# Optimization experiments

Hardware: AMD Instinct MI355X
Metric: run time of the kernel (lower is better)

## Reference

```python
import jax, jax.numpy as jnp
import numpy as np

N_SRC0, N_DST0, N_DST1 = 400000, 200000, 100000
E0, E1 = 3200000, 1600000
IN_FEATS, H_FEATS, NUM_CLASSES, NUM_CELL_TYPES = 128, 256, 8, 24


def setup_inputs() -> dict:
    key = jax.random.key(0)
    ks = jax.random.split(key, 12)
    feats = jax.random.normal(ks[0], (N_SRC0, IN_FEATS), dtype=jnp.float32)
    cell_ids = jax.random.randint(ks[1], (N_SRC0,), 0, NUM_CELL_TYPES)
    x = jnp.concatenate([cell_ids.astype(jnp.float32)[:, None], feats], axis=1)  # [N,129]
    src0 = jax.random.randint(ks[2], (E0,), 0, N_SRC0, dtype=jnp.int32)
    dst0 = jax.random.randint(ks[3], (E0,), 0, N_DST0, dtype=jnp.int32)
    src1 = jax.random.randint(ks[4], (E1,), 0, N_DST0, dtype=jnp.int32)
    dst1 = jax.random.randint(ks[5], (E1,), 0, N_DST1, dtype=jnp.int32)
    s = 1.0 / np.sqrt(IN_FEATS)
    s2 = 1.0 / np.sqrt(H_FEATS)
    return {
        "x": x,
        "src0": src0, "dst0": dst0, "src1": src1, "dst1": dst1,
        "n_dst0": N_DST0, "n_dst1": N_DST1,
        "emb": jax.random.normal(ks[6], (NUM_CELL_TYPES, IN_FEATS), dtype=jnp.float32),
        "W_self1": jax.random.normal(ks[7], (IN_FEATS, H_FEATS), dtype=jnp.float32) * s,
        "W_neigh1": jax.random.normal(ks[8], (IN_FEATS, H_FEATS), dtype=jnp.float32) * s,
        "b1": jnp.zeros((H_FEATS,), dtype=jnp.float32),
        "W_self2": jax.random.normal(ks[9], (H_FEATS, NUM_CLASSES), dtype=jnp.float32) * s2,
        "W_neigh2": jax.random.normal(ks[10], (H_FEATS, NUM_CLASSES), dtype=jnp.float32) * s2,
        "b2": jnp.zeros((NUM_CLASSES,), dtype=jnp.float32),
    }


def _sage_mean(h_src, h_dst, src, dst, n_dst, W_self, W_neigh, b):
    # gather src features along edges, mean-reduce onto dst nodes
    msg = h_src[src]                                                # [E, d]
    agg = jax.ops.segment_sum(msg, dst, num_segments=n_dst)        # [n_dst, d]
    deg = jax.ops.segment_sum(jnp.ones_like(dst, dtype=h_src.dtype), dst, num_segments=n_dst)
    agg = agg / jnp.maximum(deg, 1.0)[:, None]
    return h_dst @ W_self + agg @ W_neigh + b


def reference(x, src0, dst0, src1, dst1, n_dst0, n_dst1,
              emb, W_self1, W_neigh1, b1, W_self2, W_neigh2, b2):
    cell_ids = x[:, 0].astype(jnp.int32)
    feat = x[:, 1:]
    h = feat * jax.nn.sigmoid(emb[cell_ids])  # embedding-gated features; dropout = identity (eval)
    h_dst = h[:n_dst0]
    h1 = jax.nn.relu(_sage_mean(h, h_dst, src0, dst0, n_dst0, W_self1, W_neigh1, b1))
    h1_dst = h1[:n_dst1]
    out = _sage_mean(h1, h1_dst, src1, dst1, n_dst1, W_self2, W_neigh2, b2)
    return out
```

## Files before the change

kernel.cpp:

```cpp
#include <hip/hip_runtime.h>

typedef unsigned int uint;
typedef unsigned short ushort;
typedef __attribute__((ext_vector_type(8))) short short8;
typedef __attribute__((ext_vector_type(4))) float f32x4;

__device__ __forceinline__ float bflo(uint u) { return __uint_as_float(u << 16); }
__device__ __forceinline__ float bfhi(uint u) { return __uint_as_float(u & 0xffff0000u); }
__device__ __forceinline__ ushort f2bf(float f) {
    uint u = __float_as_uint(f);
    u += 0x7fffu + ((u >> 16) & 1u);
    return (ushort)(u >> 16);
}
__device__ __forceinline__ uint pack2(float a, float b) {
    return (uint)f2bf(a) | ((uint)f2bf(b) << 16);
}
__device__ __forceinline__ float sigm(float e) { return 1.0f / (1.0f + __expf(-e)); }

#define ND0 200000
#define ND1 100000
#define INF 128
#define HF  256
#define BCAP 24576
#define GSTRIDE 16

__global__ __launch_bounds__(256) void gate_k(const float* __restrict__ x,
                                              const float* __restrict__ emb,
                                              ushort* __restrict__ h, int nnodes) {
    int tid  = blockIdx.x * 256 + threadIdx.x;
    int node = tid >> 4, tq = tid & 15;
    if (node >= nnodes) return;
    const float* xr = x + (size_t)node * 129;
    int cell = (int)xr[0];
    int f0 = tq * 8;
    const float* er = emb + cell * INF + f0;
    float4 e0 = *(const float4*)er;
    float4 e1 = *(const float4*)(er + 4);
    float v[8];
    __builtin_memcpy(&v[0], xr + 1 + f0, 16);
    __builtin_memcpy(&v[4], xr + 5 + f0, 16);
    uint4 o;
    o.x = pack2(v[0] * sigm(e0.x), v[1] * sigm(e0.y));
    o.y = pack2(v[2] * sigm(e0.z), v[3] * sigm(e0.w));
    o.z = pack2(v[4] * sigm(e1.x), v[5] * sigm(e1.y));
    o.w = pack2(v[6] * sigm(e1.z), v[7] * sigm(e1.w));
    *(uint4*)(h + (size_t)node * INF + f0) = o;
}

#define SCAN_B 1024
__global__ __launch_bounds__(256) void scan1_k(const int* __restrict__ in,
                                               int* __restrict__ out,
                                               int* __restrict__ bsum, int n) {
    __shared__ int tmp[256];
    int t = threadIdx.x;
    int base = blockIdx.x * SCAN_B;
    int v[4], s = 0;
#pragma unroll
    for (int q = 0; q < 4; ++q) {
        int idx = base + t * 4 + q;
        v[q] = (idx < n) ? ((in[idx] + 3) & ~3) : 0;
        s += v[q];
    }
    tmp[t] = s; __syncthreads();
    for (int off = 1; off < 256; off <<= 1) {
        int xv = (t >= off) ? tmp[t - off] : 0; __syncthreads();
        tmp[t] += xv; __syncthreads();
    }
    int excl = tmp[t] - s;
#pragma unroll
    for (int q = 0; q < 4; ++q) {
        int idx = base + t * 4 + q;
        if (idx < n) out[idx] = excl;
        excl += v[q];
    }
    if (t == 255) bsum[blockIdx.x] = tmp[255];
}

__global__ __launch_bounds__(256) void scan2_k(int* __restrict__ bsum, int nb) {
    __shared__ int tmp[256];
    int t = threadIdx.x;
    int s = (t < nb) ? bsum[t] : 0;
    tmp[t] = s; __syncthreads();
    for (int off = 1; off < 256; off <<= 1) {
        int xv = (t >= off) ? tmp[t - off] : 0; __syncthreads();
        tmp[t] += xv; __syncthreads();
    }
    if (t < nb) bsum[t] = tmp[t] - s;
}

__global__ __launch_bounds__(256) void scan3_k(int* __restrict__ row_start,
                                               const int* __restrict__ bsum, int n) {
    int i = blockIdx.x * blockDim.x + threadIdx.x;
    if (i < n) row_start[i] += bsum[i >> 10];
}

#define CHUNK_A 2048
__global__ __launch_bounds__(256) void binA_k(const int* __restrict__ src,
                                              const int* __restrict__ dst,
                                              uint* __restrict__ pairs,
                                              int* __restrict__ gcur,
                                              int* __restrict__ cnt, int E) {
    __shared__ int hist[256];
    __shared__ int base[256];
    int t = threadIdx.x;
    for (int c0 = blockIdx.x * CHUNK_A; c0 < E; c0 += gridDim.x * CHUNK_A) {
        int n = min(CHUNK_A, E - c0);
        hist[t] = 0;
        __syncthreads();
        int i0 = t * 8;
        uint meta[8];
        if (i0 + 8 <= n) {
            int4 da = *(const int4*)(dst + c0 + i0);
            int4 db = *(const int4*)(dst + c0 + i0 + 4);
            int dv[8] = { da.x, da.y, da.z, da.w, db.x, db.y, db.z, db.w };
#pragma unroll
            for (int q = 0; q < 8; ++q) {
                int d = dv[q];
                atomicAdd(&cnt[d], 1);
                int b = d >> 10;
                int r = atomicAdd(&hist[b], 1);
                meta[q] = ((uint)b << 21) | ((uint)r << 10) | (uint)(d & 1023);
            }
        } else {
#pragma unroll
            for (int q = 0; q < 8; ++q) {
                int i = i0 + q;
                if (i < n) {
                    int d = dst[c0 + i];
                    atomicAdd(&cnt[d], 1);
                    int b = d >> 10;
                    int r = atomicAdd(&hist[b], 1);
                    meta[q] = ((uint)b << 21) | ((uint)r << 10) | (uint)(d & 1023);
                } else meta[q] = 0xFFFFFFFFu;
            }
        }
        __syncthreads();
        base[t] = hist[t] ? atomicAdd(&gcur[t * GSTRIDE], hist[t]) : 0;
        __syncthreads();
        if (i0 + 8 <= n) {
            int4 sa = *(const int4*)(src + c0 + i0);
            int4 sb = *(const int4*)(src + c0 + i0 + 4);
            int sv[8] = { sa.x, sa.y, sa.z, sa.w, sb.x, sb.y, sb.z, sb.w };
#pragma unroll
            for (int q = 0; q < 8; ++q) {
                uint m = meta[q];
                uint b = m >> 21;
                uint p = (uint)base[b] + ((m >> 10) & 2047u);
                pairs[(size_t)b * BCAP + p] = ((uint)sv[q] << 10) | (m & 1023u);
            }
        } else {
#pragma unroll
            for (int q = 0; q < 8; ++q) {
                uint m = meta[q];
                if (m != 0xFFFFFFFFu) {
                    uint b = m >> 21;
                    uint p = (uint)base[b] + ((m >> 10) & 2047u);
                    pairs[(size_t)b * BCAP + p] = ((uint)src[c0 + i0 + q] << 10) | (m & 1023u);
                }
            }
        }
        __syncthreads();
    }
}

__global__ __launch_bounds__(1024) void binB_k(const uint* __restrict__ pairs,
                                               const int* __restrict__ gcur,
                                               const int* __restrict__ row_start,
                                               int* __restrict__ csr, int nd, int zrow) {
    __shared__ int cur[1024];
    int b = blockIdx.x, t = threadIdx.x;
    int dbase = b << 10;
    cur[t] = (dbase + t < nd) ? row_start[dbase + t] : 0;
    __syncthreads();
    int ne = gcur[b * GSTRIDE];
    const uint* bp = pairs + (size_t)b * BCAP;
    for (int i = t; i < ne; i += 1024) {
        uint e = bp[i];
        int p = atomicAdd(&cur[e & 1023], 1);
        csr[p] = (int)(e >> 10);
    }
    __syncthreads();
    if (dbase + t < nd) {
        int pe = cur[t];
        int pad = (-(pe - row_start[dbase + t])) & 3;
        for (int q = 0; q < pad; ++q) csr[pe + q] = zrow;
    }
}

__global__ __launch_bounds__(256) void gather4_k(const int* __restrict__ csr,
                                                 const int* __restrict__ row_start,
                                                 const int* __restrict__ cnt,
                                                 const ushort* __restrict__ hsrc,
                                                 uint* __restrict__ aggm, int nrows) {
    int w    = (blockIdx.x * blockDim.x + threadIdx.x) >> 6;
    int lane = threadIdx.x & 63;
    if (w >= nrows) return;
    int beg = row_start[w], c = cnt[w];
    int end = beg + ((c + 3) & ~3);
    const uint* hb = (const uint*)hsrc;
    float a0 = 0.f, a1 = 0.f;
    for (int j = beg; j < end; j += 4) {
        int4 s4 = *(const int4*)(csr + j);
        uint u0 = hb[(size_t)s4.x * 64 + lane];
        uint u1 = hb[(size_t)s4.y * 64 + lane];
        uint u2 = hb[(size_t)s4.z * 64 + lane];
        uint u3 = hb[(size_t)s4.w * 64 + lane];
        a0 += (bflo(u0) + bflo(u1)) + (bflo(u2) + bflo(u3));
        a1 += (bfhi(u0) + bfhi(u1)) + (bfhi(u2) + bfhi(u3));
    }
    float inv = 1.0f / fmaxf((float)c, 1.0f);
    aggm[(size_t)w * 64 + lane] = pack2(a0 * inv, a1 * inv);
}

__global__ __launch_bounds__(256) void wconv_k(const float* __restrict__ Ws,
                                               const float* __restrict__ Wn,
                                               uint* __restrict__ Wb) {
    int tid  = blockIdx.x * 256 + threadIdx.x;
    int lane = tid & 63, nf = (tid >> 6) & 15, ks = tid >> 10;
    int n  = nf * 16 + (lane & 15);
    int k0 = ks * 32 + ((lane >> 4) << 3);
    uint o[4];
#pragma unroll
    for (int p = 0; p < 4; ++p) {
        int k = k0 + 2 * p;
        float a = (k < 128)     ? Ws[(size_t)k * HF + n]       : Wn[(size_t)(k - 128) * HF + n];
        float b = (k + 1 < 128) ? Ws[(size_t)(k + 1) * HF + n] : Wn[(size_t)(k - 127) * HF + n];
        o[p] = pack2(a, b);
    }
    uint4 v = { o[0], o[1], o[2], o[3] };
    *(uint4*)(Wb + (size_t)tid * 4) = v;
}

__global__ __launch_bounds__(256) void wpack2_k(const float* __restrict__ Ws2,
                                                const float* __restrict__ Wn2,
                                                uint* __restrict__ Wb2) {
    int tid = blockIdx.x * 256 + threadIdx.x;
    if (tid >= 512) return;
    int lane = tid & 63, ks = tid >> 6;
    int n  = lane & 15;
    int k0 = ks * 32 + ((lane >> 4) << 3);
    const float* W = (n < 8) ? Wn2 : Ws2;
    int c = n & 7;
    uint o[4];
#pragma unroll
    for (int p = 0; p < 4; ++p) {
        int k = k0 + 2 * p;
        o[p] = pack2(W[(size_t)k * 8 + c], W[(size_t)(k + 1) * 8 + c]);
    }
    uint4 v = { o[0], o[1], o[2], o[3] };
    *(uint4*)(Wb2 + (size_t)tid * 4) = v;
}

__global__ __launch_bounds__(256) void layer1_mfma_k(const uint* __restrict__ hb,
                                                     const uint* __restrict__ aggm,
                                                     const uint* __restrict__ Wb,
                                                     const uint* __restrict__ Wb2,
                                                     const float* __restrict__ b1,
                                                     float* __restrict__ z,
                                                     float* __restrict__ out, int nd1) {
    __shared__ uint lds[64 * 132];
    int t = threadIdx.x, lane = t & 63, wid = t >> 6;
    int quad = lane >> 4, l16 = lane & 15;
    int r0 = blockIdx.x * 64;

#pragma unroll
    for (int it = 0; it < 8; ++it) {
        int i = t + it * 256;
        int r = i >> 5, u4 = i & 31;
        const uint* src = (u4 < 16) ? (hb + (size_t)(r0 + r) * 64 + u4 * 4)
                                    : (aggm + (size_t)(r0 + r) * 64 + (u4 - 16) * 4);
        *(uint4*)&lds[r * 132 + u4 * 4] = *(const uint4*)src;
    }

    float bias[4];
#pragma unroll
    for (int i = 0; i < 4; ++i) bias[i] = b1[wid * 64 + i * 16 + l16];
    f32x4 acc[4][4];
#pragma unroll
    for (int mf = 0; mf < 4; ++mf)
#pragma unroll
        for (int i = 0; i < 4; ++i)
            acc[mf][i] = (f32x4){ bias[i], bias[i], bias[i], bias[i] };

    __syncthreads();

#pragma unroll
    for (int ks = 0; ks < 8; ++ks) {
        short8 bfr[4];
#pragma unroll
        for (int i = 0; i < 4; ++i) {
            int nf = wid * 4 + i;
            bfr[i] = *(const short8*)(Wb + (size_t)((ks * 16 + nf) * 64 + lane) * 4);
        }
        short8 afr[4];
#pragma unroll
        for (int mf = 0; mf < 4; ++mf) {
            int r = mf * 16 + l16;
            afr[mf] = *(const short8*)&lds[r * 132 + ks * 16 + quad * 4];
        }
#pragma unroll
        for (int mf = 0; mf < 4; ++mf)
#pragma unroll
            for (int i = 0; i < 4; ++i)
                acc[mf][i] = __builtin_amdgcn_mfma_f32_16x16x32_bf16(afr[mf], bfr[i],
                                                                     acc[mf][i], 0, 0, 0);
    }

    __syncthreads();
    ushort* st = (ushort*)lds;
#pragma unroll
    for (int mf = 0; mf < 4; ++mf)
#pragma unroll
        for (int i = 0; i < 4; ++i) {
            int col = wid * 64 + i * 16 + l16;
#pragma unroll
            for (int reg = 0; reg < 4; ++reg) {
                int row = mf * 16 + quad * 4 + reg;
                st[row * 264 + col] = f2bf(fmaxf(acc[mf][i][reg], 0.0f));
            }
        }
    __syncthreads();

    f32x4 zacc = (f32x4){ 0.f, 0.f, 0.f, 0.f };
    int rloc = wid * 16 + l16;
#pragma unroll
    for (int ks = 0; ks < 8; ++ks) {
        short8 a = *(const short8*)&lds[rloc * 132 + ks * 16 + quad * 4];
        short8 b = *(const short8*)(Wb2 + (size_t)(ks * 64 + lane) * 4);
        zacc = __builtin_amdgcn_mfma_f32_16x16x32_bf16(a, b, zacc, 0, 0, 0);
    }
#pragma unroll
    for (int reg = 0; reg < 4; ++reg) {
        int r = r0 + wid * 16 + quad * 4 + reg;
        if (l16 < 8) z[(size_t)r * 8 + l16] = zacc[reg];
        else if (r < nd1) out[(size_t)r * 8 + (l16 - 8)] = zacc[reg];
    }
}

__global__ __launch_bounds__(256) void gz_k(const int* __restrict__ csr,
                                            const int* __restrict__ row_start,
                                            const int* __restrict__ cnt,
                                            const float* __restrict__ z,
                                            const float* __restrict__ b2,
                                            float* __restrict__ out, int nrows) {
    int tid = blockIdx.x * 256 + threadIdx.x;
    int d = tid >> 3, c = tid & 7;
    if (d >= nrows) return;
    int beg = row_start[d], n = cnt[d];
    int end = beg + ((n + 3) & ~3);
    float a = 0.f;
    for (int j = beg; j < end; j += 4) {
        int4 s4 = *(const int4*)(csr + j);
        a += z[(size_t)s4.x * 8 + c] + z[(size_t)s4.y * 8 + c]
           + z[(size_t)s4.z * 8 + c] + z[(size_t)s4.w * 8 + c];
    }
    float inv = 1.0f / fmaxf((float)n, 1.0f);
    out[(size_t)d * 8 + c] += a * inv + b2[c];
}

extern "C" void kernel_launch(void* const* d_in, const int* in_sizes, int n_in,
                              void* d_out, int out_size, void* d_ws, size_t ws_size,
                              hipStream_t stream) {
    const float* x    = (const float*)d_in[0];
    const int*   src0 = (const int*)d_in[1];
    const int*   dst0 = (const int*)d_in[2];
    const int*   src1 = (const int*)d_in[3];
    const int*   dst1 = (const int*)d_in[4];
    const float* emb  = (const float*)d_in[7];
    const float* Ws1  = (const float*)d_in[8];
    const float* Wn1  = (const float*)d_in[9];
    const float* b1   = (const float*)d_in[10];
    const float* Ws2  = (const float*)d_in[11];
    const float* Wn2  = (const float*)d_in[12];
    const float* b2   = (const float*)d_in[13];
    int E0 = in_sizes[1];
    int E1 = in_sizes[3];
    int nsrc = in_sizes[0] / 129;

    char* p = (char*)d_ws;
    ushort* h         = (ushort*)p;  p += ((size_t)nsrc + 1) * INF * 2;
    uint*   aggm      = (uint*)p;    p += (size_t)ND0 * 64 * 4;
    int*    csr       = (int*)p;     p += ((size_t)E0 + 3 * (size_t)ND0 + 16) * 4;
    int*    cnt       = (int*)p;     p += (size_t)ND0 * 4;
    int*    row_start = (int*)p;     p += (size_t)ND0 * 4;
    int*    bsum      = (int*)p;     p += 256 * 4;
    int*    gcur      = (int*)p;     p += 256 * GSTRIDE * 4;
    uint*   Wb        = (uint*)p;    p += 8192 * 16;
    uint*   Wb2       = (uint*)p;    p += 512 * 16;
    float*  z         = (float*)p;   p += ((size_t)ND0 + 1) * 8 * 4;
    uint*   pairs     = aggm;

    int ZR0 = nsrc;
    int ZR1 = ND0;

    hipMemsetAsync(cnt, 0, (size_t)ND0 * 4, stream);
    hipMemsetAsync(gcur, 0, 256 * GSTRIDE * 4, stream);
    hipMemsetAsync(h + (size_t)ZR0 * INF, 0, INF * 2, stream);
    gate_k<<<(nsrc * 16 + 255) / 256, 256, 0, stream>>>(x, emb, h, nsrc);
    wconv_k<<<32, 256, 0, stream>>>(Ws1, Wn1, Wb);
    wpack2_k<<<2, 256, 0, stream>>>(Ws2, Wn2, Wb2);
    int nb0 = (ND0 + SCAN_B - 1) / SCAN_B;
    int ch0 = (E0 + CHUNK_A - 1) / CHUNK_A;
    binA_k<<<min(ch0, 2048), 256, 0, stream>>>(src0, dst0, pairs, gcur, cnt, E0);
    scan1_k<<<nb0, 256, 0, stream>>>(cnt, row_start, bsum, ND0);
    scan2_k<<<1, 256, 0, stream>>>(bsum, nb0);
    scan3_k<<<(ND0 + 255) / 256, 256, 0, stream>>>(row_start, bsum, ND0);
    binB_k<<<nb0, 1024, 0, stream>>>(pairs, gcur, row_start, csr, ND0, ZR0);
    gather4_k<<<(ND0 + 3) / 4, 256, 0, stream>>>(csr, row_start, cnt, h, aggm, ND0);
    layer1_mfma_k<<<ND0 / 64, 256, 0, stream>>>((const uint*)h, aggm, Wb, Wb2, b1,
                                                z, (float*)d_out, ND1);

    hipMemsetAsync(cnt, 0, (size_t)ND1 * 4, stream);
    hipMemsetAsync(gcur, 0, 256 * GSTRIDE * 4, stream);
    hipMemsetAsync(z + (size_t)ZR1 * 8, 0, 8 * 4, stream);
    int nb1 = (ND1 + SCAN_B - 1) / SCAN_B;
    int ch1 = (E1 + CHUNK_A - 1) / CHUNK_A;
    binA_k<<<min(ch1, 2048), 256, 0, stream>>>(src1, dst1, pairs, gcur, cnt, E1);
    scan1_k<<<nb1, 256, 0, stream>>>(cnt, row_start, bsum, ND1);
    scan2_k<<<1, 256, 0, stream>>>(bsum, nb1);
    scan3_k<<<(ND1 + 255) / 256, 256, 0, stream>>>(row_start, bsum, ND1);
    binB_k<<<nb1, 1024, 0, stream>>>(pairs, gcur, row_start, csr, ND1, ZR1);
    gz_k<<<(ND1 * 8 + 255) / 256, 256, 0, stream>>>(csr, row_start, cnt, z, b2,
                                                    (float*)d_out, ND1);
}
```

Before: 855.1 us.

## Stage edge binning in LDS and compute per-node degrees in a separate pass

The binning kernel now stages edges per 1024-node bucket in shared memory and flushes them in 16-aligned chunks padded with sentinels. Overflow past a small per-bucket capacity falls back to per-edge global atomics. The global per-destination degree atomics are removed. Degrees are instead counted by a new per-bucket kernel using shared-memory histograms, which also drops the cnt memsets. This trades scattered global atomics and stores for an extra pass over the pairs buffer and larger bucket capacity with sentinel padding.

```diff
diff --git a/kernel.cpp b/kernel.cpp
--- a/kernel.cpp
+++ b/kernel.cpp
@@ -21,8 +21,11 @@
 #define ND1 100000
 #define INF 128
 #define HF  256
-#define BCAP 24576
+#define BCAP 32768
 #define GSTRIDE 16
+#define NBKT 200
+#define CAP_A 48
+#define SENT 0xFFFFFFFFu
 
 __global__ __launch_bounds__(256) void gate_k(const float* __restrict__ x,
                                               const float* __restrict__ emb,
@@ -94,73 +97,86 @@
     if (i < n) row_start[i] += bsum[i >> 10];
 }
 
-#define CHUNK_A 2048
+template <int CPT>
 __global__ __launch_bounds__(256) void binA_k(const int* __restrict__ src,
                                               const int* __restrict__ dst,
                                               uint* __restrict__ pairs,
-                                              int* __restrict__ gcur,
-                                              int* __restrict__ cnt, int E) {
-    __shared__ int hist[256];
-    __shared__ int base[256];
+                                              int* __restrict__ gcur, int E) {
+    __shared__ int  lcur[NBKT];
+    __shared__ uint stage[NBKT][CAP_A];
     int t = threadIdx.x;
-    for (int c0 = blockIdx.x * CHUNK_A; c0 < E; c0 += gridDim.x * CHUNK_A) {
-        int n = min(CHUNK_A, E - c0);
-        hist[t] = 0;
-        __syncthreads();
-        int i0 = t * 8;
-        uint meta[8];
-        if (i0 + 8 <= n) {
-            int4 da = *(const int4*)(dst + c0 + i0);
-            int4 db = *(const int4*)(dst + c0 + i0 + 4);
-            int dv[8] = { da.x, da.y, da.z, da.w, db.x, db.y, db.z, db.w };
-#pragma unroll
-            for (int q = 0; q < 8; ++q) {
+    int c0 = blockIdx.x * (256 * CPT);
+    int n = min(256 * CPT, E - c0);
+    for (int i = t; i < NBKT; i += 256) lcur[i] = 0;
+    __syncthreads();
+
+    int i0 = t * CPT;
+    if (i0 + CPT <= n) {
+#pragma unroll
+        for (int v = 0; v < CPT / 4; ++v) {
+            int4 d4 = *(const int4*)(dst + c0 + i0 + v * 4);
+            int4 s4 = *(const int4*)(src + c0 + i0 + v * 4);
+            int dv[4] = { d4.x, d4.y, d4.z, d4.w };
+            int sv[4] = { s4.x, s4.y, s4.z, s4.w };
+#pragma unroll
+            for (int q = 0; q < 4; ++q) {
                 int d = dv[q];
-                atomicAdd(&cnt[d], 1);
                 int b = d >> 10;
-                int r = atomicAdd(&hist[b], 1);
-                meta[q] = ((uint)b << 21) | ((uint)r << 10) | (uint)(d & 1023);
-            }
-        } else {
-#pragma unroll
-            for (int q = 0; q < 8; ++q) {
-                int i = i0 + q;
-                if (i < n) {
-                    int d = dst[c0 + i];
-                    atomicAdd(&cnt[d], 1);
-                    int b = d >> 10;
-                    int r = atomicAdd(&hist[b], 1);
-                    meta[q] = ((uint)b << 21) | ((uint)r << 10) | (uint)(d & 1023);
-                } else meta[q] = 0xFFFFFFFFu;
-            }
-        }
-        __syncthreads();
-        base[t] = hist[t] ? atomicAdd(&gcur[t * GSTRIDE], hist[t]) : 0;
-        __syncthreads();
-        if (i0 + 8 <= n) {
-            int4 sa = *(const int4*)(src + c0 + i0);
-            int4 sb = *(const int4*)(src + c0 + i0 + 4);
-            int sv[8] = { sa.x, sa.y, sa.z, sa.w, sb.x, sb.y, sb.z, sb.w };
-#pragma unroll
-            for (int q = 0; q < 8; ++q) {
-                uint m = meta[q];
-                uint b = m >> 21;
-                uint p = (uint)base[b] + ((m >> 10) & 2047u);
-                pairs[(size_t)b * BCAP + p] = ((uint)sv[q] << 10) | (m & 1023u);
-            }
-        } else {
-#pragma unroll
-            for (int q = 0; q < 8; ++q) {
-                uint m = meta[q];
-                if (m != 0xFFFFFFFFu) {
-                    uint b = m >> 21;
-                    uint p = (uint)base[b] + ((m >> 10) & 2047u);
-                    pairs[(size_t)b * BCAP + p] = ((uint)src[c0 + i0 + q] << 10) | (m & 1023u);
+                uint e = ((uint)sv[q] << 10) | (uint)(d & 1023);
+                int r = atomicAdd(&lcur[b], 1);
+                if (r < CAP_A) stage[b][r] = e;
+                else {
+                    int p = atomicAdd(&gcur[b * GSTRIDE], 1);
+                    pairs[(size_t)b * BCAP + p] = e;
                 }
             }
         }
-        __syncthreads();
-    }
+    } else {
+        for (int q = 0; q < CPT; ++q) {
+            int i = i0 + q;
+            if (i >= n) break;
+            int d = dst[c0 + i];
+            int b = d >> 10;
+            uint e = ((uint)src[c0 + i] << 10) | (uint)(d & 1023);
+            int r = atomicAdd(&lcur[b], 1);
+            if (r < CAP_A) stage[b][r] = e;
+            else {
+                int p = atomicAdd(&gcur[b * GSTRIDE], 1);
+                pairs[(size_t)b * BCAP + p] = e;
+            }
+        }
+    }
+    __syncthreads();
+
+    int wid = t >> 6, lane = t & 63;
+    for (int b = wid; b < NBKT; b += 4) {
+        int cnt = min(lcur[b], CAP_A);
+        if (cnt == 0) continue;
+        int padded = (cnt + 15) & ~15;
+        int base;
+        if (lane == 0) base = atomicAdd(&gcur[b * GSTRIDE], padded);
+        base = __shfl(base, 0);
+        if (lane < padded)
+            pairs[(size_t)b * BCAP + base + lane] = (lane < cnt) ? stage[b][lane] : SENT;
+    }
+}
+
+__global__ __launch_bounds__(1024) void binC_k(const uint* __restrict__ pairs,
+                                               const int* __restrict__ gcur,
+                                               int* __restrict__ cnt, int nd) {
+    __shared__ int h[1024];
+    int b = blockIdx.x, t = threadIdx.x;
+    h[t] = 0;
+    __syncthreads();
+    int ne = gcur[b * GSTRIDE];
+    const uint* bp = pairs + (size_t)b * BCAP;
+    for (int i = t; i < ne; i += 1024) {
+        uint e = bp[i];
+        if (e != SENT) atomicAdd(&h[e & 1023], 1);
+    }
+    __syncthreads();
+    int d = (b << 10) + t;
+    if (d < nd) cnt[d] = h[t];
 }
 
 __global__ __launch_bounds__(1024) void binB_k(const uint* __restrict__ pairs,
@@ -176,6 +192,7 @@
     const uint* bp = pairs + (size_t)b * BCAP;
     for (int i = t; i < ne; i += 1024) {
         uint e = bp[i];
+        if (e == SENT) continue;
         int p = atomicAdd(&cur[e & 1023], 1);
         csr[p] = (int)(e >> 10);
     }
@@ -393,15 +410,15 @@
     int ZR0 = nsrc;
     int ZR1 = ND0;
 
-    hipMemsetAsync(cnt, 0, (size_t)ND0 * 4, stream);
     hipMemsetAsync(gcur, 0, 256 * GSTRIDE * 4, stream);
     hipMemsetAsync(h + (size_t)ZR0 * INF, 0, INF * 2, stream);
     gate_k<<<(nsrc * 16 + 255) / 256, 256, 0, stream>>>(x, emb, h, nsrc);
     wconv_k<<<32, 256, 0, stream>>>(Ws1, Wn1, Wb);
     wpack2_k<<<2, 256, 0, stream>>>(Ws2, Wn2, Wb2);
     int nb0 = (ND0 + SCAN_B - 1) / SCAN_B;
-    int ch0 = (E0 + CHUNK_A - 1) / CHUNK_A;
-    binA_k<<<min(ch0, 2048), 256, 0, stream>>>(src0, dst0, pairs, gcur, cnt, E0);
+    int ch0 = (E0 + 256 * 16 - 1) / (256 * 16);
+    binA_k<16><<<ch0, 256, 0, stream>>>(src0, dst0, pairs, gcur, E0);
+    binC_k<<<nb0, 1024, 0, stream>>>(pairs, gcur, cnt, ND0);
     scan1_k<<<nb0, 256, 0, stream>>>(cnt, row_start, bsum, ND0);
     scan2_k<<<1, 256, 0, stream>>>(bsum, nb0);
     scan3_k<<<(ND0 + 255) / 256, 256, 0, stream>>>(row_start, bsum, ND0);
@@ -410,12 +427,12 @@
     layer1_mfma_k<<<ND0 / 64, 256, 0, stream>>>((const uint*)h, aggm, Wb, Wb2, b1,
                                                 z, (float*)d_out, ND1);
 
-    hipMemsetAsync(cnt, 0, (size_t)ND1 * 4, stream);
     hipMemsetAsync(gcur, 0, 256 * GSTRIDE * 4, stream);
     hipMemsetAsync(z + (size_t)ZR1 * 8, 0, 8 * 4, stream);
     int nb1 = (ND1 + SCAN_B - 1) / SCAN_B;
-    int ch1 = (E1 + CHUNK_A - 1) / CHUNK_A;
-    binA_k<<<min(ch1, 2048), 256, 0, stream>>>(src1, dst1, pairs, gcur, cnt, E1);
+    int ch1 = (E1 + 256 * 8 - 1) / (256 * 8);
+    binA_k<8><<<ch1, 256, 0, stream>>>(src1, dst1, pairs, gcur, E1);
+    binC_k<<<nb1, 1024, 0, stream>>>(pairs, gcur, cnt, ND1);
     scan1_k<<<nb1, 256, 0, stream>>>(cnt, row_start, bsum, ND1);
     scan2_k<<<1, 256, 0, stream>>>(bsum, nb1);
     scan3_k<<<(ND1 + 255) / 256, 256, 0, stream>>>(row_start, bsum, ND1);
```

Result: faster. 733.4 us (-14.2%).
